# Performance work log

Measured on AMD Instinct MI355X. Metric: run time of the kernel, lower is better.

The kernel has to match this reference:

```python
import jax, jax.numpy as jnp
import numpy as np

B, T, D_IN, H, OUT = 256, 512, 128, 256, 128


def setup_inputs() -> dict:
    key = jax.random.key(0)
    ks = jax.random.split(key, 10)
    s_in = 1.0 / np.sqrt(H)
    inp = {
        "x": jax.random.normal(ks[0], (B, T, D_IN), dtype=jnp.float32),
        # layer 0 (PyTorch LSTM gate order: i, f, g, o along 4H)
        "W_ih0": jax.random.uniform(ks[1], (4 * H, D_IN), minval=-s_in, maxval=s_in),
        "W_hh0": jax.random.uniform(ks[2], (4 * H, H), minval=-s_in, maxval=s_in),
        "b_ih0": jax.random.uniform(ks[3], (4 * H,), minval=-s_in, maxval=s_in),
        "b_hh0": jax.random.uniform(ks[4], (4 * H,), minval=-s_in, maxval=s_in),
        # layer 1
        "W_ih1": jax.random.uniform(ks[5], (4 * H, H), minval=-s_in, maxval=s_in),
        "W_hh1": jax.random.uniform(ks[6], (4 * H, H), minval=-s_in, maxval=s_in),
        "b_ih1": jax.random.uniform(ks[7], (4 * H,), minval=-s_in, maxval=s_in),
        "b_hh1": jax.random.uniform(ks[8], (4 * H,), minval=-s_in, maxval=s_in),
        # fc head (bias=False)
        "W_fc": jax.random.uniform(ks[9], (OUT, H), minval=-s_in, maxval=s_in),
    }
    return inp


def _lstm_layer(x_seq, W_ih, W_hh, b_ih, b_hh):
    # x_seq: [B, T, D]; precompute input projection once (big GEMM),
    # leave only the small h@W_hh GEMM inside the sequential scan.
    b, t = x_seq.shape[0], x_seq.shape[1]
    h_dim = W_hh.shape[1]
    x_proj = jnp.einsum('btd,gd->btg', x_seq, W_ih) + b_ih + b_hh  # [B,T,4H]

    def step(carry, xt):
        h, c = carry
        gates = xt + h @ W_hh.T  # [B,4H]
        i, f, g, o = jnp.split(gates, 4, axis=-1)
        i = jax.nn.sigmoid(i)
        f = jax.nn.sigmoid(f)
        g = jnp.tanh(g)
        o = jax.nn.sigmoid(o)
        c = f * c + i * g
        h = o * jnp.tanh(c)
        return (h, c), h

    init = (jnp.zeros((b, h_dim), x_seq.dtype), jnp.zeros((b, h_dim), x_seq.dtype))
    _, hs = jax.lax.scan(step, init, jnp.swapaxes(x_proj, 0, 1))  # hs: [T,B,H]
    return jnp.swapaxes(hs, 0, 1)  # [B,T,H]


def reference(x, W_ih0, W_hh0, b_ih0, b_hh0, W_ih1, W_hh1, b_ih1, b_hh1, W_fc):
    h0 = _lstm_layer(x, W_ih0, W_hh0, b_ih0, b_hh0)   # [B,T,H]
    h1 = _lstm_layer(h0, W_ih1, W_hh1, b_ih1, b_hh1)  # [B,T,H]
    last = h1[:, -1, :]                               # [B,H]
    return last @ W_fc.T                              # [B,OUT]
```

## Files before the change

### kernel.cpp

```cpp
#include <hip/hip_runtime.h>
#include <stdint.h>

#define T_   512
#define H_   256
#define OUTD 128

typedef unsigned long long u64;
typedef __attribute__((ext_vector_type(8))) short s8v;
typedef __attribute__((ext_vector_type(4))) float f4v;

__device__ __forceinline__ f4v mfma16x16x32(s8v a, s8v b, f4v c) {
  return __builtin_amdgcn_mfma_f32_16x16x32_bf16(a, b, c, 0, 0, 0);
}

__device__ __forceinline__ void split_bf16(float f, short &hi, short &lo) {
  unsigned u  = __float_as_uint(f);
  unsigned uh = u & 0xffff0000u;
  hi = (short)(uh >> 16);
  float r = f - __uint_as_float(uh);
  unsigned ur = __float_as_uint(r);
  lo = (short)((ur + 0x7fffu + ((ur >> 16) & 1u)) >> 16);
}

__device__ __forceinline__ unsigned pack_hilo(float f) {
  short hi, lo; split_bf16(f, hi, lo);
  return ((unsigned)(unsigned short)hi << 16) | (unsigned)(unsigned short)lo;
}

__device__ __forceinline__ float sig_(float x) { return 1.f / (1.f + __expf(-x)); }
__device__ __forceinline__ float th_(float x)  { float e = __expf(2.f * x); return 1.f - 2.f / (e + 1.f); }

struct SMem {
  short xhi[16][264], xlo[16][264];
  short hhi[16][264], hlo[16][264];
  float gl[4][16][17];
  float bias[64];
};

template <int LAYER>
__device__ __forceinline__ void lstm_body(
    SMem* sm,
    const float* __restrict__ xin,
    const float* __restrict__ Wih, const float* __restrict__ Whh,
    const float* __restrict__ bih, const float* __restrict__ bhh,
    u64* bx_x,
    u64* bx_own,
    unsigned* rflag,
    float* h1l,
    int g, int mem)
{
  constexpr int KX  = (LAYER == 0) ? 128 : 256;
  constexpr int NKX = KX / 32;
  const int tid = threadIdx.x;
  const int w = tid >> 6, lane = tid & 63, n = lane & 15, q = lane >> 4;
  const int bb = tid >> 4, uu = tid & 15;
  const int B0 = g * 16, U0 = mem * 16;

  s8v wxh[NKX], wxl[NKX], whhh[8], whhl[8];
  {
    const int row = w * 256 + U0 + n;
    #pragma unroll
    for (int kf = 0; kf < NKX; ++kf) {
      s8v vh, vl;
      #pragma unroll
      for (int j = 0; j < 8; ++j) { short hi, lo; split_bf16(Wih[row * KX + kf * 32 + q * 8 + j], hi, lo); vh[j] = hi; vl[j] = lo; }
      wxh[kf] = vh; wxl[kf] = vl;
    }
    #pragma unroll
    for (int kf = 0; kf < 8; ++kf) {
      s8v vh, vl;
      #pragma unroll
      for (int j = 0; j < 8; ++j) { short hi, lo; split_bf16(Whh[row * 256 + kf * 32 + q * 8 + j], hi, lo); vh[j] = hi; vl[j] = lo; }
      whhh[kf] = vh; whhl[kf] = vl;
    }
  }
  if (tid < 64) {
    int gate = tid >> 4, u = tid & 15;
    int grow = gate * 256 + U0 + u;
    sm->bias[tid] = bih[grow] + bhh[grow];
  }

  u64* own = bx_own + (size_t)g * 2 * 4096;
  u64* src = (LAYER == 1) ? (bx_x + (size_t)g * 2 * 4096) : nullptr;
  unsigned* rfg    = rflag + g * 256;
  unsigned* rfself = rfg + mem * 16;

  float c = 0.f;

  for (int s = 0; s < T_; ++s) {
    float xv[8];
    if (LAYER == 0) {
      const float* px = xin + ((size_t)(B0 + bb) * T_ + s) * 128 + uu * 8;
      float4 v0 = *(const float4*)px, v1 = *(const float4*)(px + 4);
      xv[0] = v0.x; xv[1] = v0.y; xv[2] = v0.z; xv[3] = v0.w;
      xv[4] = v1.x; xv[5] = v1.y; xv[6] = v1.z; xv[7] = v1.w;
    }

    if (LAYER == 1) {
      const u64* pbx = src + (size_t)(s & 1) * 4096;
      const unsigned xtag = (unsigned)(s + 1);
      u64 xv64[16]; int it = 0;
      for (;;) {
        bool ok = true;
        #pragma unroll
        for (int i = 0; i < 16; ++i)
          xv64[i] = __hip_atomic_load(&pbx[i * 256 + tid], __ATOMIC_RELAXED, __HIP_MEMORY_SCOPE_AGENT);
        #pragma unroll
        for (int i = 0; i < 16; ++i) ok &= ((unsigned)(xv64[i] >> 32) == xtag);
        if (ok) break;
        if (++it >= 50000) break;
        __builtin_amdgcn_s_sleep(1);
      }
      #pragma unroll
      for (int i = 0; i < 16; ++i) {
        unsigned d = (unsigned)xv64[i];
        sm->xhi[i][tid] = (short)(d >> 16);
        sm->xlo[i][tid] = (short)(d & 0xffffu);
      }
    }

    if (s > 0) {
      const u64* pbh = own + (size_t)((s - 1) & 1) * 4096;
      const unsigned htag = (unsigned)s;
      u64 hv64[16]; int it = 0;
      for (;;) {
        bool ok = true;
        #pragma unroll
        for (int i = 0; i < 16; ++i)
          hv64[i] = __hip_atomic_load(&pbh[i * 256 + tid], __ATOMIC_RELAXED, __HIP_MEMORY_SCOPE_AGENT);
        #pragma unroll
        for (int i = 0; i < 16; ++i) ok &= ((unsigned)(hv64[i] >> 32) == htag);
        if (ok) break;
        if (++it >= 50000) break;
        __builtin_amdgcn_s_sleep(1);
      }
      #pragma unroll
      for (int i = 0; i < 16; ++i) {
        unsigned d = (unsigned)hv64[i];
        sm->hhi[i][tid] = (short)(d >> 16);
        sm->hlo[i][tid] = (short)(d & 0xffffu);
      }
    } else {
      #pragma unroll
      for (int i = 0; i < 16; ++i) { sm->hhi[i][tid] = 0; sm->hlo[i][tid] = 0; }
    }

    if (LAYER == 0) {
      s8v vh, vl;
      #pragma unroll
      for (int j = 0; j < 8; ++j) { short hi, lo; split_bf16(xv[j], hi, lo); vh[j] = hi; vl[j] = lo; }
      *(s8v*)&sm->xhi[bb][uu * 8] = vh;
      *(s8v*)&sm->xlo[bb][uu * 8] = vl;
    }
    __syncthreads();

    if (LAYER == 1 && tid == 0)
      __hip_atomic_store(rfself, (unsigned)(s + 1), __ATOMIC_RELAXED, __HIP_MEMORY_SCOPE_AGENT);

    f4v a0 = {0.f, 0.f, 0.f, 0.f}, a1 = a0, a2 = a0;
    #pragma unroll
    for (int kf = 0; kf < NKX; ++kf) {
      s8v ah = *(const s8v*)&sm->xhi[n][kf * 32 + q * 8];
      s8v al = *(const s8v*)&sm->xlo[n][kf * 32 + q * 8];
      a0 = mfma16x16x32(ah, wxh[kf], a0);
      a1 = mfma16x16x32(al, wxh[kf], a1);
      a2 = mfma16x16x32(ah, wxl[kf], a2);
    }
    #pragma unroll
    for (int kf = 0; kf < 8; ++kf) {
      s8v ah = *(const s8v*)&sm->hhi[n][kf * 32 + q * 8];
      s8v al = *(const s8v*)&sm->hlo[n][kf * 32 + q * 8];
      a0 = mfma16x16x32(ah, whhh[kf], a0);
      a1 = mfma16x16x32(al, whhh[kf], a1);
      a2 = mfma16x16x32(ah, whhl[kf], a2);
    }
    f4v D = a0 + (a1 + a2);
    #pragma unroll
    for (int r = 0; r < 4; ++r) sm->gl[w][q * 4 + r][n] = D[r];
    __syncthreads();

    float pi = sm->gl[0][bb][uu] + sm->bias[uu];
    float pf = sm->gl[1][bb][uu] + sm->bias[16 + uu];
    float pg = sm->gl[2][bb][uu] + sm->bias[32 + uu];
    float po = sm->gl[3][bb][uu] + sm->bias[48 + uu];
    float ig = sig_(pi), fg = sig_(pf), gg = th_(pg), og = sig_(po);
    c = fg * c + ig * gg;
    float h = og * th_(c);

    if (LAYER == 0) {
      if (s >= 2 && w == 0) {
        const unsigned tgt = (unsigned)(s - 1); int it = 0;
        for (;;) {
          unsigned v = (lane < 16)
            ? __hip_atomic_load(&rfg[lane * 16], __ATOMIC_RELAXED, __HIP_MEMORY_SCOPE_AGENT)
            : tgt;
          if (__all((int)(v >= tgt))) break;
          if (++it >= 50000) break;
          __builtin_amdgcn_s_sleep(1);
        }
      }
      __syncthreads();
    }

    u64 val = ((u64)(unsigned)(s + 1) << 32) | (u64)pack_hilo(h);
    __hip_atomic_store(&own[(size_t)(s & 1) * 4096 + bb * 256 + U0 + uu], val,
                       __ATOMIC_RELAXED, __HIP_MEMORY_SCOPE_AGENT);

    if (LAYER == 1 && s == T_ - 1)
      h1l[(B0 + bb) * H_ + U0 + uu] = h;
  }
}

__global__ __launch_bounds__(256, 2) void lstm_fused(
    const float* __restrict__ x,
    const float* __restrict__ Wih0, const float* __restrict__ Whh0,
    const float* __restrict__ bih0, const float* __restrict__ bhh0,
    const float* __restrict__ Wih1, const float* __restrict__ Whh1,
    const float* __restrict__ bih1, const float* __restrict__ bhh1,
    u64* bx0, u64* bx1, unsigned* rflag, float* h1l)
{
  __shared__ SMem sm;
  const int bid = blockIdx.x;
  if (bid < 256) {
    lstm_body<0>(&sm, x, Wih0, Whh0, bih0, bhh0, nullptr, bx0, rflag, nullptr,
                 bid >> 4, bid & 15);
  } else {
    const int b = bid - 256;
    lstm_body<1>(&sm, nullptr, Wih1, Whh1, bih1, bhh1, bx0, bx1, rflag, h1l,
                 b >> 4, b & 15);
  }
}

__global__ void fc_kernel(const float* __restrict__ h1l, const float* __restrict__ Wfc,
                          float* __restrict__ out) {
  __shared__ float hs[H_];
  const int b = blockIdx.x, o = threadIdx.x;
  hs[o]       = h1l[b * H_ + o];
  hs[o + 128] = h1l[b * H_ + o + 128];
  __syncthreads();
  float acc = 0.f;
  #pragma unroll 8
  for (int u = 0; u < H_; u += 4) {
    float4 wv = *(const float4*)&Wfc[o * H_ + u];
    acc += wv.x * hs[u] + wv.y * hs[u + 1] + wv.z * hs[u + 2] + wv.w * hs[u + 3];
  }
  out[b * OUTD + o] = acc;
}

extern "C" void kernel_launch(void* const* d_in, const int* in_sizes, int n_in,
                              void* d_out, int out_size, void* d_ws, size_t ws_size,
                              hipStream_t stream) {
  const float* x    = (const float*)d_in[0];
  const float* Wih0 = (const float*)d_in[1];
  const float* Whh0 = (const float*)d_in[2];
  const float* bih0 = (const float*)d_in[3];
  const float* bhh0 = (const float*)d_in[4];
  const float* Wih1 = (const float*)d_in[5];
  const float* Whh1 = (const float*)d_in[6];
  const float* bih1 = (const float*)d_in[7];
  const float* bhh1 = (const float*)d_in[8];
  const float* Wfc  = (const float*)d_in[9];

  u64*      bx0   = (u64*)d_ws;
  u64*      bx1   = bx0 + 131072;
  unsigned* rflag = (unsigned*)(bx1 + 131072);
  float*    h1l   = (float*)(rflag + 4096);

  hipMemsetAsync(rflag, 0, 4096 * sizeof(unsigned), stream);

  lstm_fused<<<512, 256, 0, stream>>>(x, Wih0, Whh0, bih0, bhh0,
                                      Wih1, Whh1, bih1, bhh1,
                                      bx0, bx1, rflag, h1l);
  fc_kernel<<<256, 128, 0, stream>>>(h1l, Wfc, (float*)d_out);
}
```

Measured before the change: 2.709 ms.

## Deepen inter-layer ring buffer and merge polling to loosen layer sync

```diff
diff --git a/kernel.cpp b/kernel.cpp
--- a/kernel.cpp
+++ b/kernel.cpp
@@ -1,9 +1,10 @@
 #include <hip/hip_runtime.h>
 #include <stdint.h>
 
-#define T_   512
-#define H_   256
-#define OUTD 128
+#define T_    512
+#define H_    256
+#define OUTD  128
+#define DEPTH 8
 
 typedef unsigned long long u64;
 typedef __attribute__((ext_vector_type(8))) short s8v;
@@ -35,6 +36,7 @@
   short hhi[16][264], hlo[16][264];
   float gl[4][16][17];
   float bias[64];
+  unsigned rfmin;
 };
 
 template <int LAYER>
@@ -43,10 +45,7 @@
     const float* __restrict__ xin,
     const float* __restrict__ Wih, const float* __restrict__ Whh,
     const float* __restrict__ bih, const float* __restrict__ bhh,
-    u64* bx_x,
-    u64* bx_own,
-    unsigned* rflag,
-    float* h1l,
+    u64* bx_x, u64* bx_own, unsigned* rflag, float* h1l,
     int g, int mem)
 {
   constexpr int KX  = (LAYER == 0) ? 128 : 256;
@@ -80,12 +79,13 @@
     sm->bias[tid] = bih[grow] + bhh[grow];
   }
 
-  u64* own = bx_own + (size_t)g * 2 * 4096;
-  u64* src = (LAYER == 1) ? (bx_x + (size_t)g * 2 * 4096) : nullptr;
+  u64* own = bx_own + (size_t)g * DEPTH * 4096;
+  u64* src = (LAYER == 1) ? (bx_x + (size_t)g * DEPTH * 4096) : nullptr;
   unsigned* rfg    = rflag + g * 256;
   unsigned* rfself = rfg + mem * 16;
 
   float c = 0.f;
+  unsigned rf_cached = 0;
 
   for (int s = 0; s < T_; ++s) {
     float xv[8];
@@ -97,19 +97,50 @@
     }
 
     if (LAYER == 1) {
-      const u64* pbx = src + (size_t)(s & 1) * 4096;
+      const u64* pbx = src + (size_t)(s % DEPTH) * 4096;
       const unsigned xtag = (unsigned)(s + 1);
-      u64 xv64[16]; int it = 0;
-      for (;;) {
-        bool ok = true;
+      u64 xv64[16];
+      if (s > 0) {
+        const u64* pbh = own + (size_t)((s - 1) % DEPTH) * 4096;
+        const unsigned htag = (unsigned)s;
+        u64 hv64[16]; int it = 0;
+        for (;;) {
+          bool ok = true;
+          #pragma unroll
+          for (int i = 0; i < 16; ++i)
+            xv64[i] = __hip_atomic_load(&pbx[i * 256 + tid], __ATOMIC_RELAXED, __HIP_MEMORY_SCOPE_AGENT);
+          #pragma unroll
+          for (int i = 0; i < 16; ++i)
+            hv64[i] = __hip_atomic_load(&pbh[i * 256 + tid], __ATOMIC_RELAXED, __HIP_MEMORY_SCOPE_AGENT);
+          #pragma unroll
+          for (int i = 0; i < 16; ++i) ok &= ((unsigned)(xv64[i] >> 32) == xtag);
+          #pragma unroll
+          for (int i = 0; i < 16; ++i) ok &= ((unsigned)(hv64[i] >> 32) == htag);
+          if (ok) break;
+          if (++it >= 20000) break;
+          __builtin_amdgcn_s_sleep(1);
+        }
         #pragma unroll
-        for (int i = 0; i < 16; ++i)
-          xv64[i] = __hip_atomic_load(&pbx[i * 256 + tid], __ATOMIC_RELAXED, __HIP_MEMORY_SCOPE_AGENT);
+        for (int i = 0; i < 16; ++i) {
+          unsigned d = (unsigned)hv64[i];
+          sm->hhi[i][tid] = (short)(d >> 16);
+          sm->hlo[i][tid] = (short)(d & 0xffffu);
+        }
+      } else {
+        int it = 0;
+        for (;;) {
+          bool ok = true;
+          #pragma unroll
+          for (int i = 0; i < 16; ++i)
+            xv64[i] = __hip_atomic_load(&pbx[i * 256 + tid], __ATOMIC_RELAXED, __HIP_MEMORY_SCOPE_AGENT);
+          #pragma unroll
+          for (int i = 0; i < 16; ++i) ok &= ((unsigned)(xv64[i] >> 32) == xtag);
+          if (ok) break;
+          if (++it >= 20000) break;
+          __builtin_amdgcn_s_sleep(1);
+        }
         #pragma unroll
-        for (int i = 0; i < 16; ++i) ok &= ((unsigned)(xv64[i] >> 32) == xtag);
-        if (ok) break;
-        if (++it >= 50000) break;
-        __builtin_amdgcn_s_sleep(1);
+        for (int i = 0; i < 16; ++i) { sm->hhi[i][tid] = 0; sm->hlo[i][tid] = 0; }
       }
       #pragma unroll
       for (int i = 0; i < 16; ++i) {
@@ -117,35 +148,32 @@
         sm->xhi[i][tid] = (short)(d >> 16);
         sm->xlo[i][tid] = (short)(d & 0xffffu);
       }
-    }
-
-    if (s > 0) {
-      const u64* pbh = own + (size_t)((s - 1) & 1) * 4096;
-      const unsigned htag = (unsigned)s;
-      u64 hv64[16]; int it = 0;
-      for (;;) {
-        bool ok = true;
+    } else {
+      if (s > 0) {
+        const u64* pbh = own + (size_t)((s - 1) % DEPTH) * 4096;
+        const unsigned htag = (unsigned)s;
+        u64 hv64[16]; int it = 0;
+        for (;;) {
+          bool ok = true;
+          #pragma unroll
+          for (int i = 0; i < 16; ++i)
+            hv64[i] = __hip_atomic_load(&pbh[i * 256 + tid], __ATOMIC_RELAXED, __HIP_MEMORY_SCOPE_AGENT);
+          #pragma unroll
+          for (int i = 0; i < 16; ++i) ok &= ((unsigned)(hv64[i] >> 32) == htag);
+          if (ok) break;
+          if (++it >= 20000) break;
+          __builtin_amdgcn_s_sleep(1);
+        }
         #pragma unroll
-        for (int i = 0; i < 16; ++i)
-          hv64[i] = __hip_atomic_load(&pbh[i * 256 + tid], __ATOMIC_RELAXED, __HIP_MEMORY_SCOPE_AGENT);
+        for (int i = 0; i < 16; ++i) {
+          unsigned d = (unsigned)hv64[i];
+          sm->hhi[i][tid] = (short)(d >> 16);
+          sm->hlo[i][tid] = (short)(d & 0xffffu);
+        }
+      } else {
         #pragma unroll
-        for (int i = 0; i < 16; ++i) ok &= ((unsigned)(hv64[i] >> 32) == htag);
-        if (ok) break;
-        if (++it >= 50000) break;
-        __builtin_amdgcn_s_sleep(1);
+        for (int i = 0; i < 16; ++i) { sm->hhi[i][tid] = 0; sm->hlo[i][tid] = 0; }
       }
-      #pragma unroll
-      for (int i = 0; i < 16; ++i) {
-        unsigned d = (unsigned)hv64[i];
-        sm->hhi[i][tid] = (short)(d >> 16);
-        sm->hlo[i][tid] = (short)(d & 0xffffu);
-      }
-    } else {
-      #pragma unroll
-      for (int i = 0; i < 16; ++i) { sm->hhi[i][tid] = 0; sm->hlo[i][tid] = 0; }
-    }
-
-    if (LAYER == 0) {
       s8v vh, vl;
       #pragma unroll
       for (int j = 0; j < 8; ++j) { short hi, lo; split_bf16(xv[j], hi, lo); vh[j] = hi; vl[j] = lo; }
@@ -177,7 +205,32 @@
     f4v D = a0 + (a1 + a2);
     #pragma unroll
     for (int r = 0; r < 4; ++r) sm->gl[w][q * 4 + r][n] = D[r];
+
+    bool polled = false;
+    if (LAYER == 0 && s >= DEPTH) {
+      const unsigned tgt = (unsigned)(s - DEPTH + 1);
+      polled = (rf_cached < tgt);
+      if (polled && w == 0) {
+        unsigned mn; int it = 0;
+        for (;;) {
+          unsigned v = (lane < 16)
+            ? __hip_atomic_load(&rfg[lane * 16], __ATOMIC_RELAXED, __HIP_MEMORY_SCOPE_AGENT)
+            : 0xffffffffu;
+          mn = v;
+          #pragma unroll
+          for (int off = 8; off; off >>= 1) {
+            unsigned o = __shfl_xor(mn, off, 16);
+            mn = (o < mn) ? o : mn;
+          }
+          if (mn >= tgt) break;
+          if (++it >= 20000) break;
+          __builtin_amdgcn_s_sleep(1);
+        }
+        if (lane == 0) sm->rfmin = mn;
+      }
+    }
     __syncthreads();
+    if (polled) rf_cached = sm->rfmin;
 
     float pi = sm->gl[0][bb][uu] + sm->bias[uu];
     float pf = sm->gl[1][bb][uu] + sm->bias[16 + uu];
@@ -187,23 +240,8 @@
     c = fg * c + ig * gg;
     float h = og * th_(c);
 
-    if (LAYER == 0) {
-      if (s >= 2 && w == 0) {
-        const unsigned tgt = (unsigned)(s - 1); int it = 0;
-        for (;;) {
-          unsigned v = (lane < 16)
-            ? __hip_atomic_load(&rfg[lane * 16], __ATOMIC_RELAXED, __HIP_MEMORY_SCOPE_AGENT)
-            : tgt;
-          if (__all((int)(v >= tgt))) break;
-          if (++it >= 50000) break;
-          __builtin_amdgcn_s_sleep(1);
-        }
-      }
-      __syncthreads();
-    }
-
     u64 val = ((u64)(unsigned)(s + 1) << 32) | (u64)pack_hilo(h);
-    __hip_atomic_store(&own[(size_t)(s & 1) * 4096 + bb * 256 + U0 + uu], val,
+    __hip_atomic_store(&own[(size_t)(s % DEPTH) * 4096 + bb * 256 + U0 + uu], val,
                        __ATOMIC_RELAXED, __HIP_MEMORY_SCOPE_AGENT);
 
     if (LAYER == 1 && s == T_ - 1)
@@ -262,8 +300,8 @@
   const float* Wfc  = (const float*)d_in[9];
 
   u64*      bx0   = (u64*)d_ws;
-  u64*      bx1   = bx0 + 131072;
-  unsigned* rflag = (unsigned*)(bx1 + 131072);
+  u64*      bx1   = bx0 + 16 * DEPTH * 4096;
+  unsigned* rflag = (unsigned*)(bx1 + 16 * DEPTH * 4096);
   float*    h1l   = (float*)(rflag + 4096);
 
   hipMemsetAsync(rflag, 0, 4096 * sizeof(unsigned), stream);
```

Result: slower. 4.131 ms (+52.5%).
